# Performance work log

Hardware: AMD Instinct MI355X
Metric: run time of the kernel (lower is better)

Reference implementation:

```python
import jax, jax.numpy as jnp
import numpy as np


def setup_inputs() -> dict:
    key = jax.random.key(0)
    ks = jax.random.split(key, 4)
    B, N, D, C = 8, 32768, 128, 64
    H = D // 2
    features = jax.random.normal(ks[0], (B, N, D), dtype=jnp.float32)
    cluster_assignments = jax.random.randint(ks[1], (B, N), 0, C)
    W1 = jax.random.normal(ks[2], (D, H), dtype=jnp.float32) * (1.0 / np.sqrt(D))
    b1 = jnp.zeros((H,), dtype=jnp.float32)
    W2 = jax.random.normal(ks[3], (H, 1), dtype=jnp.float32) * (1.0 / np.sqrt(H))
    b2 = jnp.zeros((1,), dtype=jnp.float32)
    return {"features": features, "cluster_assignments": cluster_assignments,
            "W1": W1, "b1": b1, "W2": W2, "b2": b2, "num_clusters": C}


def reference(features, cluster_assignments, W1, b1, W2, b2, num_clusters):
    # features: [B, N, D]; cluster_assignments: [B, N] ints in [0, num_clusters)
    B, N, D = features.shape
    # importance_net: Linear -> ReLU -> Linear -> Sigmoid
    h = jax.nn.relu(jnp.einsum('bnd,dh->bnh', features, W1) + b1)
    imp = jax.nn.sigmoid(jnp.einsum('bnh,ho->bno', h, W2) + b2)[..., 0]  # [B, N]

    # Fused per-(batch, cluster) softmax-weighted segment sum.
    num_seg = B * num_clusters
    seg = (cluster_assignments + num_clusters * jnp.arange(B)[:, None]).reshape(-1)  # [B*N]
    imp_f = imp.reshape(-1)
    # stable softmax within each segment
    seg_max = jax.ops.segment_max(imp_f, seg, num_segments=num_seg)  # -inf for empty
    e = jnp.exp(imp_f - seg_max[seg])
    denom = jax.ops.segment_sum(e, seg, num_segments=num_seg)
    w = e / denom[seg]  # [B*N]
    out = jax.ops.segment_sum(features.reshape(-1, D) * w[:, None], seg,
                              num_segments=num_seg)  # empty clusters -> zeros
    return out.reshape(B, num_clusters, D)
```

## Files before the change

kernel.cpp:

```cpp
#include <hip/hip_runtime.h>
#include <hip/hip_bf16.h>


#define B_ 8
#define N_ 32768
#define D_ 128
#define C_ 64
#define H_ 64

#define NTHREADS 512
#define NWAVES 8
#define ROWS_PER_BLOCK 512
#define NBLOCKS ((B_ * N_) / ROWS_PER_BLOCK)
#define SLICES (NBLOCKS / B_)
#define NSS 4
#define RST 136
#define W1S 136

typedef float f32x4 __attribute__((ext_vector_type(4)));
typedef short s16x8 __attribute__((ext_vector_type(8)));

__device__ __forceinline__ short bf16rne(float x) {
    unsigned u = __float_as_uint(x);
    u = (u + 0x7FFFu + ((u >> 16) & 1u)) >> 16;
    return (short)u;
}

__device__ __forceinline__ s16x8 pk8(float4 a, float4 b) {
    union { s16x8 v; __hip_bfloat162 h[4]; } u;
    u.h[0] = __float22bfloat162_rn(make_float2(a.x, a.y));
    u.h[1] = __float22bfloat162_rn(make_float2(a.z, a.w));
    u.h[2] = __float22bfloat162_rn(make_float2(b.x, b.y));
    u.h[3] = __float22bfloat162_rn(make_float2(b.z, b.w));
    return u.v;
}

template <bool USE_WS>
__global__ __launch_bounds__(NTHREADS, 4)
void ca_fused_kernel(const float* __restrict__ features,
                     const int* __restrict__ ca,
                     const float* __restrict__ b1,
                     const float* __restrict__ W2,
                     const float* __restrict__ b2,
                     const float* __restrict__ W1,
                     float* __restrict__ out_sums,
                     float* __restrict__ denoms,
                     float* __restrict__ pout,
                     float* __restrict__ pden)
{
    __shared__ __align__(16) unsigned short ft[D_ * RST];
    __shared__ __align__(16) unsigned short w1l[H_ * W1S];
    __shared__ __align__(16) unsigned long long ce[128];

    const int tid  = threadIdx.x;
    const int lane = tid & 63;
    const int wave = tid >> 6;
    const int m    = lane & 15;
    const int kb   = lane >> 4;
    const int bidx = blockIdx.x;
    const int b    = bidx / SLICES;
    const int row_blk0 = bidx * ROWS_PER_BLOCK;

    for (int i = tid; i < H_ * D_; i += NTHREADS) {
        const int k = i >> 6, h = i & 63;
        w1l[h * W1S + k] = (unsigned short)bf16rne(W1[i]);
    }

    float b1v[4], w2v[4];
#pragma unroll
    for (int nt = 0; nt < 4; ++nt) {
        b1v[nt] = b1[nt * 16 + m];
        w2v[nt] = W2[nt * 16 + m];
    }
    const float b2v = b2[0];

    const int CH = wave >> 1;
    const int dh = wave & 1;

    f32x4 accS[4];
    f32x4 accD = (f32x4){0.f, 0.f, 0.f, 0.f};
#pragma unroll
    for (int nt = 0; nt < 4; ++nt) accS[nt] = (f32x4){0.f, 0.f, 0.f, 0.f};

    s16x8 bones;
    {
        const short o = (m == 0) ? (short)0x3F80 : (short)0;
#pragma unroll
        for (int j = 0; j < 8; ++j) bones[j] = o;
    }

    const float* fbase = features + (long long)(row_blk0 + wave * 16 + m) * D_;
    float4 pf[8];
#pragma unroll
    for (int ks = 0; ks < 4; ++ks) {
        pf[2 * ks]     = *(const float4*)(fbase + ks * 32 + kb * 8);
        pf[2 * ks + 1] = *(const float4*)(fbase + ks * 32 + kb * 8 + 4);
    }
    int cv = 0;
    if (lane < 16) cv = ca[row_blk0 + wave * 16 + lane];

    __syncthreads();

#pragma unroll
    for (int ss = 0; ss < NSS; ++ss) {
        s16x8 af[4];
#pragma unroll
        for (int ks = 0; ks < 4; ++ks) af[ks] = pk8(pf[2 * ks], pf[2 * ks + 1]);
        const int cvc = cv;

        if (ss + 1 < NSS) {
            const float* fn = fbase + (ss + 1) * 128 * D_;
#pragma unroll
            for (int ks = 0; ks < 4; ++ks) {
                pf[2 * ks]     = *(const float4*)(fn + ks * 32 + kb * 8);
                pf[2 * ks + 1] = *(const float4*)(fn + ks * 32 + kb * 8 + 4);
            }
            if (lane < 16) cv = ca[row_blk0 + (ss + 1) * 128 + wave * 16 + lane];
        }

        const int r = wave * 16 + m;
#pragma unroll
        for (int ks = 0; ks < 4; ++ks)
#pragma unroll
            for (int j = 0; j < 8; ++j)
                ft[(ks * 32 + kb * 8 + j) * RST + r] = (unsigned short)af[ks][j];

        f32x4 hacc[4];
#pragma unroll
        for (int nt = 0; nt < 4; ++nt) hacc[nt] = (f32x4){0.f, 0.f, 0.f, 0.f};
#pragma unroll
        for (int ks = 0; ks < 4; ++ks)
#pragma unroll
            for (int nt = 0; nt < 4; ++nt) {
                const s16x8 w = *(const s16x8*)&w1l[(nt * 16 + m) * W1S +
                                                    ks * 32 + kb * 8];
                hacc[nt] = __builtin_amdgcn_mfma_f32_16x16x32_bf16(
                    af[ks], w, hacc[nt], 0, 0, 0);
            }

        float p[4];
#pragma unroll
        for (int rr = 0; rr < 4; ++rr) {
            float sv = 0.f;
#pragma unroll
            for (int nt = 0; nt < 4; ++nt)
                sv = fmaf(fmaxf(hacc[nt][rr] + b1v[nt], 0.f), w2v[nt], sv);
#pragma unroll
            for (int off = 1; off < 16; off <<= 1)
                sv += __shfl_xor(sv, off, 64);
            const float pre = sv + b2v;
            const float imp = 1.f / (1.f + __expf(-pre));
            p[rr] = __expf(imp - 1.f);
        }
        const int q = lane & 3;
        const float prov = (q == 0) ? p[0] : (q == 1) ? p[1] : (q == 2) ? p[2] : p[3];
        const int srcl = ((m >> 2) << 4) | (m & 3);
        const float eL = __shfl(prov, srcl, 64);
        if (lane < 16)
            ce[wave * 16 + lane] =
                ((unsigned long long)__float_as_uint(eL) << 32) | (unsigned)cvc;

        __syncthreads();

#pragma unroll
        for (int kg = 0; kg < 4; ++kg) {
            const ulonglong2* cp = (const ulonglong2*)&ce[kg * 32 + kb * 8];
            const ulonglong2 q0 = cp[0], q1 = cp[1], q2 = cp[2], q3 = cp[3];
            int cc[8]; short eb[8];
            cc[0] = (int)(unsigned)q0.x; eb[0] = bf16rne(__uint_as_float((unsigned)(q0.x >> 32)));
            cc[1] = (int)(unsigned)q0.y; eb[1] = bf16rne(__uint_as_float((unsigned)(q0.y >> 32)));
            cc[2] = (int)(unsigned)q1.x; eb[2] = bf16rne(__uint_as_float((unsigned)(q1.x >> 32)));
            cc[3] = (int)(unsigned)q1.y; eb[3] = bf16rne(__uint_as_float((unsigned)(q1.y >> 32)));
            cc[4] = (int)(unsigned)q2.x; eb[4] = bf16rne(__uint_as_float((unsigned)(q2.x >> 32)));
            cc[5] = (int)(unsigned)q2.y; eb[5] = bf16rne(__uint_as_float((unsigned)(q2.y >> 32)));
            cc[6] = (int)(unsigned)q3.x; eb[6] = bf16rne(__uint_as_float((unsigned)(q3.x >> 32)));
            cc[7] = (int)(unsigned)q3.y; eb[7] = bf16rne(__uint_as_float((unsigned)(q3.y >> 32)));

            s16x8 afr;
#pragma unroll
            for (int j = 0; j < 8; ++j)
                afr[j] = (cc[j] == CH * 16 + m) ? eb[j] : (short)0;

#pragma unroll
            for (int nt = 0; nt < 4; ++nt) {
                const int d0 = (dh * 4 + nt) * 16 + m;
                const s16x8 bfv = *(const s16x8*)&ft[d0 * RST + kg * 32 + kb * 8];
                accS[nt] = __builtin_amdgcn_mfma_f32_16x16x32_bf16(
                    afr, bfv, accS[nt], 0, 0, 0);
            }
            if (dh == 0)
                accD = __builtin_amdgcn_mfma_f32_16x16x32_bf16(afr, bones, accD, 0, 0, 0);
        }
        __syncthreads();
    }

#pragma unroll
    for (int nt = 0; nt < 4; ++nt)
#pragma unroll
        for (int qq = 0; qq < 4; ++qq) {
            const int idx = (CH * 16 + kb * 4 + qq) * D_ + (dh * 4 + nt) * 16 + m;
            if (USE_WS) pout[(size_t)bidx * (C_ * D_) + idx] = accS[nt][qq];
            else atomicAdd(&out_sums[b * (C_ * D_) + idx], accS[nt][qq]);
        }
    if (dh == 0 && m == 0) {
#pragma unroll
        for (int qq = 0; qq < 4; ++qq) {
            const int c = CH * 16 + kb * 4 + qq;
            if (USE_WS) pden[bidx * C_ + c] = accD[qq];
            else atomicAdd(&denoms[b * C_ + c], accD[qq]);
        }
    }
}

__global__ __launch_bounds__(512)
void ca_reduce_kernel(const float* __restrict__ pout,
                      const float* __restrict__ pden,
                      float* __restrict__ out)
{
    __shared__ float red[512];
    __shared__ float dns;

    const int bc = blockIdx.x;
    const int b  = bc >> 6;
    const int c  = bc & (C_ - 1);
    const int t  = threadIdx.x;
    const int d  = t & 127;
    const int sg = t >> 7;

    const float* pb = pout + ((size_t)(b * SLICES + sg * 16)) * (C_ * D_)
                           + c * D_ + d;
    float s = 0.f;
#pragma unroll 4
    for (int i = 0; i < 16; ++i) s += pb[(size_t)i * (C_ * D_)];
    red[t] = s;

    float dnv = 0.f;
    if (t < SLICES) dnv = pden[(b * SLICES + t) * C_ + c];
    if (t < 64) {
#pragma unroll
        for (int off = 32; off > 0; off >>= 1) dnv += __shfl_xor(dnv, off, 64);
        if (t == 0) dns = dnv;
    }
    __syncthreads();

    if (t < 128) {
        const float tot = red[t] + red[t + 128] + red[t + 256] + red[t + 384];
        const float dn = dns;
        out[(size_t)bc * D_ + t] = (dn > 0.f) ? (tot / dn) : 0.f;
    }
}

__global__ void ca_zero_kernel(float* __restrict__ out_sums,
                               float* __restrict__ denoms)
{
    const int i = blockIdx.x * blockDim.x + threadIdx.x;
    if (i < B_ * C_ * D_) out_sums[i] = 0.f;
    if (i < B_ * C_)      denoms[i] = 0.f;
}

__global__ void ca_finalize_kernel(float* __restrict__ out_sums,
                                   const float* __restrict__ denoms)
{
    const int i = blockIdx.x * blockDim.x + threadIdx.x;
    if (i >= B_ * C_ * D_) return;
    const int bc = i >> 7;
    const float den = denoms[bc];
    const float v = out_sums[i];
    out_sums[i] = (den > 0.f) ? (v / den) : 0.f;
}

extern "C" void kernel_launch(void* const* d_in, const int* in_sizes, int n_in,
                              void* d_out, int out_size, void* d_ws, size_t ws_size,
                              hipStream_t stream) {
    const float* features = (const float*)d_in[0];
    const int*   ca       = (const int*)  d_in[1];
    const float* W1       = (const float*)d_in[2];
    const float* b1       = (const float*)d_in[3];
    const float* W2       = (const float*)d_in[4];
    const float* b2       = (const float*)d_in[5];

    float* out = (float*)d_out;

    float* pden = (float*)d_ws;
    float* pout = (float*)((char*)d_ws + 131072);
    const size_t need_full = 131072 + (size_t)NBLOCKS * C_ * D_ * 4;

    if (ws_size >= need_full) {
        ca_fused_kernel<true><<<NBLOCKS, NTHREADS, 0, stream>>>(
            features, ca, b1, W2, b2, W1, nullptr, nullptr, pout, pden);
        ca_reduce_kernel<<<B_ * C_, 512, 0, stream>>>(pout, pden, out);
    } else {
        ca_zero_kernel<<<(B_ * C_ * D_ + 255) / 256, 256, 0, stream>>>(out, pden);
        ca_fused_kernel<false><<<NBLOCKS, NTHREADS, 0, stream>>>(
            features, ca, b1, W2, b2, W1, out, pden, nullptr, nullptr);
        ca_finalize_kernel<<<(B_ * C_ * D_ + 255) / 256, 256, 0, stream>>>(out, pden);
    }
}
```

Baseline: 51.21 us.

## Load transposed feature columns directly from global instead of LDS transpose buffer

Drops the shared-memory transposed feature tile. Each wave now reads its own 16-column slice of features straight from global memory, which is strided and served largely from cache, and packs it into bf16 B-operands for the segment-sum MFMA. Work is remapped so each wave owns one D-slice across all 64 clusters instead of a cluster-by-half-D split. The cluster/weight LDS exchange is compacted to 32-bit entries with pre-rounded bf16 weights. This removes the LDS transpose stores and their bank pressure, at the cost of a second, uncoalesced global read of the features and more per-lane mask construction.

```diff
diff --git a/kernel.cpp b/kernel.cpp
--- a/kernel.cpp
+++ b/kernel.cpp
@@ -14,7 +14,6 @@
 #define NBLOCKS ((B_ * N_) / ROWS_PER_BLOCK)
 #define SLICES (NBLOCKS / B_)
 #define NSS 4
-#define RST 136
 #define W1S 136
 
 typedef float f32x4 __attribute__((ext_vector_type(4)));
@@ -34,6 +33,14 @@
     u.h[3] = __float22bfloat162_rn(make_float2(b.z, b.w));
     return u.v;
 }
+
+#define PKCOL(dst, arr, base) {                                              \
+    union { s16x8 v; __hip_bfloat162 h[4]; } u_;                             \
+    u_.h[0] = __float22bfloat162_rn(make_float2(arr[(base)+0], arr[(base)+1])); \
+    u_.h[1] = __float22bfloat162_rn(make_float2(arr[(base)+2], arr[(base)+3])); \
+    u_.h[2] = __float22bfloat162_rn(make_float2(arr[(base)+4], arr[(base)+5])); \
+    u_.h[3] = __float22bfloat162_rn(make_float2(arr[(base)+6], arr[(base)+7])); \
+    dst = u_.v; }
 
 template <bool USE_WS>
 __global__ __launch_bounds__(NTHREADS, 4)
@@ -48,15 +55,15 @@
                      float* __restrict__ pout,
                      float* __restrict__ pden)
 {
-    __shared__ __align__(16) unsigned short ft[D_ * RST];
     __shared__ __align__(16) unsigned short w1l[H_ * W1S];
-    __shared__ __align__(16) unsigned long long ce[128];
+    __shared__ __align__(16) unsigned int ceu[128];
 
     const int tid  = threadIdx.x;
     const int lane = tid & 63;
     const int wave = tid >> 6;
     const int m    = lane & 15;
     const int kb   = lane >> 4;
+    const int kbase = kb * 8;
     const int bidx = blockIdx.x;
     const int b    = bidx / SLICES;
     const int row_blk0 = bidx * ROWS_PER_BLOCK;
@@ -74,13 +81,10 @@
     }
     const float b2v = b2[0];
 
-    const int CH = wave >> 1;
-    const int dh = wave & 1;
-
     f32x4 accS[4];
     f32x4 accD = (f32x4){0.f, 0.f, 0.f, 0.f};
 #pragma unroll
-    for (int nt = 0; nt < 4; ++nt) accS[nt] = (f32x4){0.f, 0.f, 0.f, 0.f};
+    for (int c4 = 0; c4 < 4; ++c4) accS[c4] = (f32x4){0.f, 0.f, 0.f, 0.f};
 
     s16x8 bones;
     {
@@ -90,11 +94,13 @@
     }
 
     const float* fbase = features + (long long)(row_blk0 + wave * 16 + m) * D_;
+    const float* fcol  = features + (long long)row_blk0 * D_ + wave * 16 + m;
+
     float4 pf[8];
 #pragma unroll
     for (int ks = 0; ks < 4; ++ks) {
-        pf[2 * ks]     = *(const float4*)(fbase + ks * 32 + kb * 8);
-        pf[2 * ks + 1] = *(const float4*)(fbase + ks * 32 + kb * 8 + 4);
+        pf[2 * ks]     = *(const float4*)(fbase + ks * 32 + kbase);
+        pf[2 * ks + 1] = *(const float4*)(fbase + ks * 32 + kbase + 4);
     }
     int cv = 0;
     if (lane < 16) cv = ca[row_blk0 + wave * 16 + lane];
@@ -112,18 +118,19 @@
             const float* fn = fbase + (ss + 1) * 128 * D_;
 #pragma unroll
             for (int ks = 0; ks < 4; ++ks) {
-                pf[2 * ks]     = *(const float4*)(fn + ks * 32 + kb * 8);
-                pf[2 * ks + 1] = *(const float4*)(fn + ks * 32 + kb * 8 + 4);
+                pf[2 * ks]     = *(const float4*)(fn + ks * 32 + kbase);
+                pf[2 * ks + 1] = *(const float4*)(fn + ks * 32 + kbase + 4);
             }
             if (lane < 16) cv = ca[row_blk0 + (ss + 1) * 128 + wave * 16 + lane];
         }
 
-        const int r = wave * 16 + m;
-#pragma unroll
-        for (int ks = 0; ks < 4; ++ks)
+        float c01[16];
+#pragma unroll
+        for (int kg = 0; kg < 2; ++kg)
 #pragma unroll
             for (int j = 0; j < 8; ++j)
-                ft[(ks * 32 + kb * 8 + j) * RST + r] = (unsigned short)af[ks][j];
+                c01[kg * 8 + j] =
+                    fcol[(size_t)(ss * 128 + kg * 32 + kbase + j) * D_];
 
         f32x4 hacc[4];
 #pragma unroll
@@ -133,7 +140,7 @@
 #pragma unroll
             for (int nt = 0; nt < 4; ++nt) {
                 const s16x8 w = *(const s16x8*)&w1l[(nt * 16 + m) * W1S +
-                                                    ks * 32 + kb * 8];
+                                                    ks * 32 + kbase];
                 hacc[nt] = __builtin_amdgcn_mfma_f32_16x16x32_bf16(
                     af[ks], w, hacc[nt], 0, 0, 0);
             }
@@ -157,55 +164,67 @@
         const int srcl = ((m >> 2) << 4) | (m & 3);
         const float eL = __shfl(prov, srcl, 64);
         if (lane < 16)
-            ce[wave * 16 + lane] =
-                ((unsigned long long)__float_as_uint(eL) << 32) | (unsigned)cvc;
+            ceu[wave * 16 + lane] =
+                ((unsigned)(unsigned short)bf16rne(eL) << 16) | (unsigned)cvc;
+
+        s16x8 bfv01[2];
+        PKCOL(bfv01[0], c01, 0);
+        PKCOL(bfv01[1], c01, 8);
+        float c23[16];
+#pragma unroll
+        for (int kg = 0; kg < 2; ++kg)
+#pragma unroll
+            for (int j = 0; j < 8; ++j)
+                c23[kg * 8 + j] =
+                    fcol[(size_t)(ss * 128 + (kg + 2) * 32 + kbase + j) * D_];
 
         __syncthreads();
 
 #pragma unroll
         for (int kg = 0; kg < 4; ++kg) {
-            const ulonglong2* cp = (const ulonglong2*)&ce[kg * 32 + kb * 8];
-            const ulonglong2 q0 = cp[0], q1 = cp[1], q2 = cp[2], q3 = cp[3];
-            int cc[8]; short eb[8];
-            cc[0] = (int)(unsigned)q0.x; eb[0] = bf16rne(__uint_as_float((unsigned)(q0.x >> 32)));
-            cc[1] = (int)(unsigned)q0.y; eb[1] = bf16rne(__uint_as_float((unsigned)(q0.y >> 32)));
-            cc[2] = (int)(unsigned)q1.x; eb[2] = bf16rne(__uint_as_float((unsigned)(q1.x >> 32)));
-            cc[3] = (int)(unsigned)q1.y; eb[3] = bf16rne(__uint_as_float((unsigned)(q1.y >> 32)));
-            cc[4] = (int)(unsigned)q2.x; eb[4] = bf16rne(__uint_as_float((unsigned)(q2.x >> 32)));
-            cc[5] = (int)(unsigned)q2.y; eb[5] = bf16rne(__uint_as_float((unsigned)(q2.y >> 32)));
-            cc[6] = (int)(unsigned)q3.x; eb[6] = bf16rne(__uint_as_float((unsigned)(q3.x >> 32)));
-            cc[7] = (int)(unsigned)q3.y; eb[7] = bf16rne(__uint_as_float((unsigned)(q3.y >> 32)));
-
-            s16x8 afr;
-#pragma unroll
-            for (int j = 0; j < 8; ++j)
-                afr[j] = (cc[j] == CH * 16 + m) ? eb[j] : (short)0;
-
-#pragma unroll
-            for (int nt = 0; nt < 4; ++nt) {
-                const int d0 = (dh * 4 + nt) * 16 + m;
-                const s16x8 bfv = *(const s16x8*)&ft[d0 * RST + kg * 32 + kb * 8];
-                accS[nt] = __builtin_amdgcn_mfma_f32_16x16x32_bf16(
-                    afr, bfv, accS[nt], 0, 0, 0);
+            const uint4* cq = (const uint4*)&ceu[kg * 32 + kbase];
+            const uint4 ua = cq[0], ub = cq[1];
+            unsigned uu[8] = {ua.x, ua.y, ua.z, ua.w, ub.x, ub.y, ub.z, ub.w};
+
+            s16x8 afr[4];
+#pragma unroll
+            for (int c4 = 0; c4 < 4; ++c4)
+#pragma unroll
+                for (int j = 0; j < 8; ++j)
+                    afr[c4][j] = ((int)(uu[j] & 0xFFu) == c4 * 16 + m)
+                                     ? (short)(uu[j] >> 16) : (short)0;
+
+            s16x8 bfv;
+            if (kg == 0)      bfv = bfv01[0];
+            else if (kg == 1) bfv = bfv01[1];
+            else if (kg == 2) { PKCOL(bfv, c23, 0); }
+            else              { PKCOL(bfv, c23, 8); }
+
+#pragma unroll
+            for (int c4 = 0; c4 < 4; ++c4)
+                accS[c4] = __builtin_amdgcn_mfma_f32_16x16x32_bf16(
+                    afr[c4], bfv, accS[c4], 0, 0, 0);
+            if (wave < 4) {
+                const s16x8 ad = (wave == 0) ? afr[0] : (wave == 1) ? afr[1]
+                                : (wave == 2) ? afr[2] : afr[3];
+                accD = __builtin_amdgcn_mfma_f32_16x16x32_bf16(ad, bones, accD, 0, 0, 0);
             }
-            if (dh == 0)
-                accD = __builtin_amdgcn_mfma_f32_16x16x32_bf16(afr, bones, accD, 0, 0, 0);
         }
         __syncthreads();
     }
 
 #pragma unroll
-    for (int nt = 0; nt < 4; ++nt)
+    for (int c4 = 0; c4 < 4; ++c4)
 #pragma unroll
         for (int qq = 0; qq < 4; ++qq) {
-            const int idx = (CH * 16 + kb * 4 + qq) * D_ + (dh * 4 + nt) * 16 + m;
-            if (USE_WS) pout[(size_t)bidx * (C_ * D_) + idx] = accS[nt][qq];
-            else atomicAdd(&out_sums[b * (C_ * D_) + idx], accS[nt][qq]);
-        }
-    if (dh == 0 && m == 0) {
+            const int idx = (c4 * 16 + kb * 4 + qq) * D_ + wave * 16 + m;
+            if (USE_WS) pout[(size_t)bidx * (C_ * D_) + idx] = accS[c4][qq];
+            else atomicAdd(&out_sums[b * (C_ * D_) + idx], accS[c4][qq]);
+        }
+    if (wave < 4 && m == 0) {
 #pragma unroll
         for (int qq = 0; qq < 4; ++qq) {
-            const int c = CH * 16 + kb * 4 + qq;
+            const int c = wave * 16 + kb * 4 + qq;
             if (USE_WS) pden[bidx * C_ + c] = accD[qq];
             else atomicAdd(&denoms[b * C_ + c], accD[qq]);
         }
```

After: 63.29 us. 1.24x slower.

## Transpose features via identity MFMA and swap GEMM operands to cut shuffles

Applied to the files above, without the earlier changes.

Replaces the scalar 2-byte LDS transpose stores with identity-matrix MFMAs that produce transposed tiles, written as packed 8-byte stores. Swaps the A/B operands of the first-layer GEMM so each lane holds hidden units for one row, reducing the per-row reduction to two cross-lane shuffles and removing the gather shuffle. Packs the bf16 weight and cluster id into 32-bit LDS entries, which shrinks the exchange buffer and the unpack work. The extra MFMAs and the bf16-rounded b1 add matrix-core work and a small change in precision.

```diff
diff --git a/kernel.cpp b/kernel.cpp
--- a/kernel.cpp
+++ b/kernel.cpp
@@ -24,6 +24,12 @@
     unsigned u = __float_as_uint(x);
     u = (u + 0x7FFFu + ((u >> 16) & 1u)) >> 16;
     return (short)u;
+}
+__device__ __forceinline__ float ubf_lo(unsigned u) {
+    return __uint_as_float(u << 16);
+}
+__device__ __forceinline__ float ubf_hi(unsigned u) {
+    return __uint_as_float(u & 0xFFFF0000u);
 }
 
 __device__ __forceinline__ s16x8 pk8(float4 a, float4 b) {
@@ -50,13 +56,14 @@
 {
     __shared__ __align__(16) unsigned short ft[D_ * RST];
     __shared__ __align__(16) unsigned short w1l[H_ * W1S];
-    __shared__ __align__(16) unsigned long long ce[128];
+    __shared__ __align__(16) unsigned int ceu[128];
 
     const int tid  = threadIdx.x;
     const int lane = tid & 63;
     const int wave = tid >> 6;
     const int m    = lane & 15;
     const int kb   = lane >> 4;
+    const int kbase = kb * 8;
     const int bidx = blockIdx.x;
     const int b    = bidx / SLICES;
     const int row_blk0 = bidx * ROWS_PER_BLOCK;
@@ -66,11 +73,20 @@
         w1l[h * W1S + k] = (unsigned short)bf16rne(W1[i]);
     }
 
-    float b1v[4], w2v[4];
-#pragma unroll
-    for (int nt = 0; nt < 4; ++nt) {
-        b1v[nt] = b1[nt * 16 + m];
-        w2v[nt] = W2[nt * 16 + m];
+    f32x4 w2v[4];
+    unsigned b1p[8];
+#pragma unroll
+    for (int c4 = 0; c4 < 4; ++c4) {
+#pragma unroll
+        for (int qq = 0; qq < 4; ++qq)
+            w2v[c4][qq] = W2[c4 * 16 + kb * 4 + qq];
+#pragma unroll
+        for (int hh = 0; hh < 2; ++hh) {
+            const int i0 = c4 * 16 + kb * 4 + hh * 2;
+            b1p[c4 * 2 + hh] =
+                ((unsigned)(unsigned short)bf16rne(b1[i0 + 1]) << 16) |
+                (unsigned)(unsigned short)bf16rne(b1[i0]);
+        }
     }
     const float b2v = b2[0];
 
@@ -88,13 +104,19 @@
 #pragma unroll
         for (int j = 0; j < 8; ++j) bones[j] = o;
     }
+    s16x8 bI0, bI1;
+#pragma unroll
+    for (int j = 0; j < 8; ++j) {
+        bI0[j] = (kbase + j == m)      ? (short)0x3F80 : (short)0;
+        bI1[j] = (kbase + j == 16 + m) ? (short)0x3F80 : (short)0;
+    }
 
     const float* fbase = features + (long long)(row_blk0 + wave * 16 + m) * D_;
     float4 pf[8];
 #pragma unroll
     for (int ks = 0; ks < 4; ++ks) {
-        pf[2 * ks]     = *(const float4*)(fbase + ks * 32 + kb * 8);
-        pf[2 * ks + 1] = *(const float4*)(fbase + ks * 32 + kb * 8 + 4);
+        pf[2 * ks]     = *(const float4*)(fbase + ks * 32 + kbase);
+        pf[2 * ks + 1] = *(const float4*)(fbase + ks * 32 + kbase + 4);
     }
     int cv = 0;
     if (lane < 16) cv = ca[row_blk0 + wave * 16 + lane];
@@ -112,79 +134,71 @@
             const float* fn = fbase + (ss + 1) * 128 * D_;
 #pragma unroll
             for (int ks = 0; ks < 4; ++ks) {
-                pf[2 * ks]     = *(const float4*)(fn + ks * 32 + kb * 8);
-                pf[2 * ks + 1] = *(const float4*)(fn + ks * 32 + kb * 8 + 4);
+                pf[2 * ks]     = *(const float4*)(fn + ks * 32 + kbase);
+                pf[2 * ks + 1] = *(const float4*)(fn + ks * 32 + kbase + 4);
             }
             if (lane < 16) cv = ca[row_blk0 + (ss + 1) * 128 + wave * 16 + lane];
         }
 
-        const int r = wave * 16 + m;
-#pragma unroll
-        for (int ks = 0; ks < 4; ++ks)
+        const int rg0 = wave * 16 + kb * 4;
+#pragma unroll
+        for (int ks = 0; ks < 4; ++ks) {
+            const f32x4 z = (f32x4){0.f, 0.f, 0.f, 0.f};
+            const f32x4 t0 = __builtin_amdgcn_mfma_f32_16x16x32_bf16(af[ks], bI0, z, 0, 0, 0);
+            const f32x4 t1 = __builtin_amdgcn_mfma_f32_16x16x32_bf16(af[ks], bI1, z, 0, 0, 0);
+            union { uint2 u; __hip_bfloat162 h[2]; } p0, p1;
+            p0.h[0] = __float22bfloat162_rn(make_float2(t0[0], t0[1]));
+            p0.h[1] = __float22bfloat162_rn(make_float2(t0[2], t0[3]));
+            p1.h[0] = __float22bfloat162_rn(make_float2(t1[0], t1[1]));
+            p1.h[1] = __float22bfloat162_rn(make_float2(t1[2], t1[3]));
+            *(uint2*)&ft[(ks * 32 + m) * RST + rg0]      = p0.u;
+            *(uint2*)&ft[(ks * 32 + 16 + m) * RST + rg0] = p1.u;
+        }
+
+        float tp = 0.f;
+#pragma unroll
+        for (int c4 = 0; c4 < 4; ++c4) {
+            f32x4 hc = (f32x4){0.f, 0.f, 0.f, 0.f};
+#pragma unroll
+            for (int ks = 0; ks < 4; ++ks) {
+                const s16x8 w = *(const s16x8*)&w1l[(c4 * 16 + m) * W1S +
+                                                    ks * 32 + kbase];
+                hc = __builtin_amdgcn_mfma_f32_16x16x32_bf16(w, af[ks], hc, 0, 0, 0);
+            }
+            const float b0 = ubf_lo(b1p[c4 * 2]),     bb1 = ubf_hi(b1p[c4 * 2]);
+            const float b2_ = ubf_lo(b1p[c4 * 2 + 1]), b3 = ubf_hi(b1p[c4 * 2 + 1]);
+            tp = fmaf(fmaxf(hc[0] + b0,  0.f), w2v[c4][0], tp);
+            tp = fmaf(fmaxf(hc[1] + bb1, 0.f), w2v[c4][1], tp);
+            tp = fmaf(fmaxf(hc[2] + b2_, 0.f), w2v[c4][2], tp);
+            tp = fmaf(fmaxf(hc[3] + b3,  0.f), w2v[c4][3], tp);
+        }
+        tp += __shfl_xor(tp, 16, 64);
+        tp += __shfl_xor(tp, 32, 64);
+        const float pre = tp + b2v;
+        const float imp = 1.f / (1.f + __expf(-pre));
+        const float e   = __expf(imp - 1.f);
+        if (lane < 16)
+            ceu[wave * 16 + lane] =
+                ((unsigned)(unsigned short)bf16rne(e) << 16) | (unsigned)cvc;
+
+        __syncthreads();
+
+#pragma unroll
+        for (int kg = 0; kg < 4; ++kg) {
+            const uint4* cq = (const uint4*)&ceu[kg * 32 + kbase];
+            const uint4 ua = cq[0], ub = cq[1];
+            const unsigned uu[8] = {ua.x, ua.y, ua.z, ua.w, ub.x, ub.y, ub.z, ub.w};
+
+            s16x8 afr;
 #pragma unroll
             for (int j = 0; j < 8; ++j)
-                ft[(ks * 32 + kb * 8 + j) * RST + r] = (unsigned short)af[ks][j];
-
-        f32x4 hacc[4];
-#pragma unroll
-        for (int nt = 0; nt < 4; ++nt) hacc[nt] = (f32x4){0.f, 0.f, 0.f, 0.f};
-#pragma unroll
-        for (int ks = 0; ks < 4; ++ks)
-#pragma unroll
-            for (int nt = 0; nt < 4; ++nt) {
-                const s16x8 w = *(const s16x8*)&w1l[(nt * 16 + m) * W1S +
-                                                    ks * 32 + kb * 8];
-                hacc[nt] = __builtin_amdgcn_mfma_f32_16x16x32_bf16(
-                    af[ks], w, hacc[nt], 0, 0, 0);
-            }
-
-        float p[4];
-#pragma unroll
-        for (int rr = 0; rr < 4; ++rr) {
-            float sv = 0.f;
-#pragma unroll
-            for (int nt = 0; nt < 4; ++nt)
-                sv = fmaf(fmaxf(hacc[nt][rr] + b1v[nt], 0.f), w2v[nt], sv);
-#pragma unroll
-            for (int off = 1; off < 16; off <<= 1)
-                sv += __shfl_xor(sv, off, 64);
-            const float pre = sv + b2v;
-            const float imp = 1.f / (1.f + __expf(-pre));
-            p[rr] = __expf(imp - 1.f);
-        }
-        const int q = lane & 3;
-        const float prov = (q == 0) ? p[0] : (q == 1) ? p[1] : (q == 2) ? p[2] : p[3];
-        const int srcl = ((m >> 2) << 4) | (m & 3);
-        const float eL = __shfl(prov, srcl, 64);
-        if (lane < 16)
-            ce[wave * 16 + lane] =
-                ((unsigned long long)__float_as_uint(eL) << 32) | (unsigned)cvc;
-
-        __syncthreads();
-
-#pragma unroll
-        for (int kg = 0; kg < 4; ++kg) {
-            const ulonglong2* cp = (const ulonglong2*)&ce[kg * 32 + kb * 8];
-            const ulonglong2 q0 = cp[0], q1 = cp[1], q2 = cp[2], q3 = cp[3];
-            int cc[8]; short eb[8];
-            cc[0] = (int)(unsigned)q0.x; eb[0] = bf16rne(__uint_as_float((unsigned)(q0.x >> 32)));
-            cc[1] = (int)(unsigned)q0.y; eb[1] = bf16rne(__uint_as_float((unsigned)(q0.y >> 32)));
-            cc[2] = (int)(unsigned)q1.x; eb[2] = bf16rne(__uint_as_float((unsigned)(q1.x >> 32)));
-            cc[3] = (int)(unsigned)q1.y; eb[3] = bf16rne(__uint_as_float((unsigned)(q1.y >> 32)));
-            cc[4] = (int)(unsigned)q2.x; eb[4] = bf16rne(__uint_as_float((unsigned)(q2.x >> 32)));
-            cc[5] = (int)(unsigned)q2.y; eb[5] = bf16rne(__uint_as_float((unsigned)(q2.y >> 32)));
-            cc[6] = (int)(unsigned)q3.x; eb[6] = bf16rne(__uint_as_float((unsigned)(q3.x >> 32)));
-            cc[7] = (int)(unsigned)q3.y; eb[7] = bf16rne(__uint_as_float((unsigned)(q3.y >> 32)));
-
-            s16x8 afr;
-#pragma unroll
-            for (int j = 0; j < 8; ++j)
-                afr[j] = (cc[j] == CH * 16 + m) ? eb[j] : (short)0;
+                afr[j] = ((int)(uu[j] & 0xFFu) == CH * 16 + m)
+                             ? (short)(uu[j] >> 16) : (short)0;
 
 #pragma unroll
             for (int nt = 0; nt < 4; ++nt) {
                 const int d0 = (dh * 4 + nt) * 16 + m;
-                const s16x8 bfv = *(const s16x8*)&ft[d0 * RST + kg * 32 + kb * 8];
+                const s16x8 bfv = *(const s16x8*)&ft[d0 * RST + kg * 32 + kbase];
                 accS[nt] = __builtin_amdgcn_mfma_f32_16x16x32_bf16(
                     afr, bfv, accS[nt], 0, 0, 0);
             }
```

Measured after the change: 55.02 us. 1.07x slower.
